# Performance work log

Measured on AMD Instinct MI355X. Metric: run time of the kernel, lower is better.

The kernel has to match this reference:

```python
import jax, jax.numpy as jnp
import numpy as np

N_NODES = 50000
N_EDGES = 800000
N_GRAPHS = 512
EPS = 1e-5
SLOPE = 0.2  # LeakyReLU negative slope in GATv2


def setup_inputs() -> dict:
    key = jax.random.key(0)
    ks = jax.random.split(key, 20)
    s = 0.1
    inp = {
        "x": jax.random.normal(ks[0], (N_NODES, 9), jnp.float32),
        "edge_attr": jax.random.normal(ks[1], (N_EDGES, 3), jnp.float32),
        "Wl0": jax.random.normal(ks[2], (9, 64), jnp.float32) * s,
        "Wr0": jax.random.normal(ks[3], (9, 64), jnp.float32) * s,
        "bl0": jnp.zeros((64,), jnp.float32),
        "br0": jnp.zeros((64,), jnp.float32),
        "We0": jax.random.normal(ks[4], (3, 64), jnp.float32) * s,
        "att0": jax.random.normal(ks[5], (64,), jnp.float32) * s,
        "bo0": jnp.zeros((64,), jnp.float32),
        "Wl": jax.random.normal(ks[6], (4, 64, 64), jnp.float32) * s,
        "Wr": jax.random.normal(ks[7], (4, 64, 64), jnp.float32) * s,
        "bl": jnp.zeros((4, 64), jnp.float32),
        "br": jnp.zeros((4, 64), jnp.float32),
        "We": jax.random.normal(ks[8], (4, 3, 64), jnp.float32) * s,
        "att": jax.random.normal(ks[9], (4, 64), jnp.float32) * s,
        "bo": jnp.zeros((4, 64), jnp.float32),
        "bn_g": jnp.ones((5, 64), jnp.float32),
        "bn_b": jnp.zeros((5, 64), jnp.float32),
        "bn_m": jnp.zeros((5, 64), jnp.float32),
        "bn_v": jax.random.uniform(ks[10], (5, 64), jnp.float32, 0.5, 1.5),
        "Wjk": jax.random.normal(ks[11], (64, 64), jnp.float32) * s,
        "bjk": jnp.zeros((64,), jnp.float32),
        "Whead": jax.random.normal(ks[12], (64, 1), jnp.float32) * s,
        "bhead": jnp.zeros((1,), jnp.float32),
        "edge_index": jax.random.randint(ks[13], (2, N_EDGES), 0, N_NODES, jnp.int32),
        "batch": jnp.sort(jax.random.randint(ks[14], (N_NODES,), 0, N_GRAPHS, jnp.int32)),
        "num_graphs": N_GRAPHS,
    }
    return inp


def gatv2_layer(h, src, dst, ea, Wl_, bl_, Wr_, br_, We_, a_, bo_, n_nodes):
    # GATv2Conv (heads=1, edge_dim) : e_ij = a . LeakyReLU(Wl h_j + Wr h_i + We e_ij)
    xl = h @ Wl_ + bl_                          # [N, 64] source transform
    xr = h @ Wr_ + br_                          # [N, 64] dest transform
    e = jax.nn.leaky_relu(xl[src] + xr[dst] + ea @ We_, SLOPE)  # [E, 64]
    logit = e @ a_                              # [E]
    m = jax.ops.segment_max(logit, dst, num_segments=n_nodes)
    m = jnp.where(jnp.isfinite(m), m, 0.0)      # empty segments -> -inf
    p = jnp.exp(logit - m[dst])
    z = jax.ops.segment_sum(p, dst, num_segments=n_nodes)
    alpha = p / jnp.maximum(z[dst], 1e-16)      # softmax over in-edges of dst
    out = jax.ops.segment_sum(alpha[:, None] * xl[src], dst, num_segments=n_nodes)
    return out + bo_


def bn_relu(h, g, b, m, v):
    # eval-mode BatchNorm1d followed by ReLU (BasicGNN: norm then act)
    return jax.nn.relu((h - m) * (g * jax.lax.rsqrt(v + EPS)) + b)


def reference(x, edge_attr, Wl0, Wr0, bl0, br0, We0, att0, bo0,
              Wl, Wr, bl, br, We, att, bo,
              bn_g, bn_b, bn_m, bn_v, Wjk, bjk, Whead, bhead,
              edge_index, batch, num_graphs):
    n = x.shape[0]
    src, dst = edge_index[0], edge_index[1]
    h = gatv2_layer(x, src, dst, edge_attr, Wl0, bl0, Wr0, br0, We0, att0, bo0, n)
    h = bn_relu(h, bn_g[0], bn_b[0], bn_m[0], bn_v[0])
    for i in range(4):
        h = gatv2_layer(h, src, dst, edge_attr, Wl[i], bl[i], Wr[i], br[i], We[i], att[i], bo[i], n)
        h = bn_relu(h, bn_g[i + 1], bn_b[i + 1], bn_m[i + 1], bn_v[i + 1])
    h = h @ Wjk + bjk                            # jk='last' output projection 64->64
    # global mean pool over graphs
    sums = jax.ops.segment_sum(h, batch, num_segments=num_graphs)          # [G, 64]
    cnt = jax.ops.segment_sum(jnp.ones((n,), h.dtype), batch, num_segments=num_graphs)
    pooled = sums / jnp.maximum(cnt, 1.0)[:, None]
    return pooled @ Whead + bhead                # [G, 1]  (dropout inactive in eval)
```

## Files before the change

### kernel.cpp

```cpp
#include <hip/hip_runtime.h>
#include <math.h>

#define N_NODES 50000
#define N_EDGES 800000
#define N_GRAPHS 512
#define SLOPE 0.2f
#define CAP 48
static constexpr float EPS_BN = 1e-5f;

typedef float v2f __attribute__((ext_vector_type(2)));


__global__ __launch_bounds__(256) void scatter_t10_kernel(
    const int* __restrict__ src, const int* __restrict__ dst,
    const float* __restrict__ ea,
    int* __restrict__ cnt, float4* __restrict__ rec,
    const float* __restrict__ x,
    const float* __restrict__ Wl0, const float* __restrict__ bl0,
    const float* __restrict__ Wr0, const float* __restrict__ br0,
    float* __restrict__ xl, float* __restrict__ xr) {
    int t = threadIdx.x;
    int e0 = blockIdx.x * 512 + t;
    int e1 = e0 + 256;
    bool v0 = e0 < N_EDGES;
    bool v1 = e1 < N_EDGES;
    int ec0 = v0 ? e0 : 0;
    int ec1 = v1 ? e1 : 0;
    int d0 = dst[ec0];
    int d1 = dst[ec1];
    int s0 = src[ec0];
    int s1 = src[ec1];
    float a00 = ea[ec0 * 3 + 0], a01 = ea[ec0 * 3 + 1], a02 = ea[ec0 * 3 + 2];
    float a10 = ea[ec1 * 3 + 0], a11 = ea[ec1 * 3 + 1], a12 = ea[ec1 * 3 + 2];
    int p0 = v0 ? atomicAdd(&cnt[d0], 1) : CAP;
    int p1 = v1 ? atomicAdd(&cnt[d1], 1) : CAP;
    if (v0 && p0 < CAP)
        rec[(size_t)d0 * CAP + p0] = make_float4(__int_as_float(s0 * 64), a00, a01, a02);
    if (v1 && p1 < CAP)
        rec[(size_t)d1 * CAP + p1] = make_float4(__int_as_float(s1 * 64), a10, a11, a12);

    int w = t >> 6;
    int k = t & 63;
    v2f wlr[9];
#pragma unroll
    for (int j = 0; j < 9; j++) wlr[j] = (v2f){Wl0[j * 64 + k], Wr0[j * 64 + k]};
    v2f bias = {bl0[k], br0[k]};
    const int NW = gridDim.x * 4;
    for (int n = blockIdx.x * 4 + w; n < N_NODES; n += NW) {
        int un = __builtin_amdgcn_readfirstlane(n);
        const float* __restrict__ hrow = x + (size_t)un * 9;
        float hb[9];
#pragma unroll
        for (int j = 0; j < 9; j++) hb[j] = hrow[j];
        v2f acc = bias;
#pragma unroll
        for (int j = 0; j < 9; j++)
            acc = __builtin_elementwise_fma((v2f){hb[j], hb[j]}, wlr[j], acc);
        xl[(size_t)un * 64 + k] = acc.x;
        xr[(size_t)un * 64 + k] = acc.y;
    }
}


__global__ __launch_bounds__(256) void transform6_kernel(
    const float* __restrict__ h,
    const float* __restrict__ Wl, const float* __restrict__ bl,
    const float* __restrict__ Wr, const float* __restrict__ br,
    float* __restrict__ xl, float* __restrict__ xr) {
    __shared__ float sAt[64][68];
    __shared__ float sB[64][128];
    int t = threadIdx.x;
    int n0 = blockIdx.x * 64;

#pragma unroll
    for (int i = 0; i < 4; i++) {
        int idx = i * 256 + t;
        int row = idx >> 4;
        int fc  = idx & 15;
        int n = n0 + row;
        float4 v = (n < N_NODES) ? *((const float4*)(h + (size_t)n * 64 + fc * 4))
                                 : make_float4(0.f, 0.f, 0.f, 0.f);
        sAt[fc * 4 + 0][row] = v.x;
        sAt[fc * 4 + 1][row] = v.y;
        sAt[fc * 4 + 2][row] = v.z;
        sAt[fc * 4 + 3][row] = v.w;
    }
#pragma unroll
    for (int i = 0; i < 8; i++) {
        int idx = i * 256 + t;
        int j  = idx >> 5;
        int fc = idx & 31;
        int c  = fc * 4;
        float4 v = (c < 64) ? *((const float4*)(Wl + j * 64 + c))
                            : *((const float4*)(Wr + j * 64 + (c - 64)));
        *((float4*)&sB[j][c]) = v;
    }
    __syncthreads();

    int tx = t & 15, ty = t >> 4;
    int c0 = tx * 4;
    float4 bls = *((const float4*)(bl + c0));
    float4 brs = *((const float4*)(br + c0));
    v2f acc[4][4];
#pragma unroll
    for (int r = 0; r < 4; r++) {
        acc[r][0] = (v2f){bls.x, bls.y};
        acc[r][1] = (v2f){bls.z, bls.w};
        acc[r][2] = (v2f){brs.x, brs.y};
        acc[r][3] = (v2f){brs.z, brs.w};
    }

#pragma unroll 4
    for (int j = 0; j < 64; j++) {
        float a0 = sAt[j][ty * 4 + 0];
        float a1 = sAt[j][ty * 4 + 1];
        float a2 = sAt[j][ty * 4 + 2];
        float a3 = sAt[j][ty * 4 + 3];
        float4 bq0 = *((const float4*)&sB[j][c0]);
        float4 bq1 = *((const float4*)&sB[j][64 + c0]);
        v2f b0 = {bq0.x, bq0.y}, b1 = {bq0.z, bq0.w};
        v2f b2 = {bq1.x, bq1.y}, b3 = {bq1.z, bq1.w};
        v2f a0v = {a0, a0}, a1v = {a1, a1}, a2v = {a2, a2}, a3v = {a3, a3};
        acc[0][0] = __builtin_elementwise_fma(a0v, b0, acc[0][0]);
        acc[0][1] = __builtin_elementwise_fma(a0v, b1, acc[0][1]);
        acc[0][2] = __builtin_elementwise_fma(a0v, b2, acc[0][2]);
        acc[0][3] = __builtin_elementwise_fma(a0v, b3, acc[0][3]);
        acc[1][0] = __builtin_elementwise_fma(a1v, b0, acc[1][0]);
        acc[1][1] = __builtin_elementwise_fma(a1v, b1, acc[1][1]);
        acc[1][2] = __builtin_elementwise_fma(a1v, b2, acc[1][2]);
        acc[1][3] = __builtin_elementwise_fma(a1v, b3, acc[1][3]);
        acc[2][0] = __builtin_elementwise_fma(a2v, b0, acc[2][0]);
        acc[2][1] = __builtin_elementwise_fma(a2v, b1, acc[2][1]);
        acc[2][2] = __builtin_elementwise_fma(a2v, b2, acc[2][2]);
        acc[2][3] = __builtin_elementwise_fma(a2v, b3, acc[2][3]);
        acc[3][0] = __builtin_elementwise_fma(a3v, b0, acc[3][0]);
        acc[3][1] = __builtin_elementwise_fma(a3v, b1, acc[3][1]);
        acc[3][2] = __builtin_elementwise_fma(a3v, b2, acc[3][2]);
        acc[3][3] = __builtin_elementwise_fma(a3v, b3, acc[3][3]);
    }

#pragma unroll
    for (int r = 0; r < 4; r++) {
        int n = n0 + ty * 4 + r;
        if (n < N_NODES) {
            *((float4*)(xl + (size_t)n * 64 + c0)) =
                make_float4(acc[r][0].x, acc[r][0].y, acc[r][1].x, acc[r][1].y);
            *((float4*)(xr + (size_t)n * 64 + c0)) =
                make_float4(acc[r][2].x, acc[r][2].y, acc[r][3].x, acc[r][3].y);
        }
    }
}


#define EDGE_T(rX, xXa, xXb, accX)                                        \
    {                                                                     \
        v2f tXa = xXa + xra, tXb = xXb + xrb;                             \
        tXa = __builtin_elementwise_fma((v2f){rX.y, rX.y}, we0a, tXa);    \
        tXb = __builtin_elementwise_fma((v2f){rX.y, rX.y}, we0b, tXb);    \
        tXa = __builtin_elementwise_fma((v2f){rX.z, rX.z}, we1a, tXa);    \
        tXb = __builtin_elementwise_fma((v2f){rX.z, rX.z}, we1b, tXb);    \
        tXa = __builtin_elementwise_fma((v2f){rX.w, rX.w}, we2a, tXa);    \
        tXb = __builtin_elementwise_fma((v2f){rX.w, rX.w}, we2b, tXb);    \
        tXa = __builtin_elementwise_max(tXa, tXa * SLOPE);                \
        tXb = __builtin_elementwise_max(tXb, tXb * SLOPE);                \
        v2f dX = ata * tXa;                                               \
        dX = __builtin_elementwise_fma(atb, tXb, dX);                     \
        accX = dX.x + dX.y;                                               \
    }

__global__ __launch_bounds__(256, 4) void gat_fused8_kernel(
    const float* __restrict__ xl, const float* __restrict__ xr,
    const float4* __restrict__ recP, const int* __restrict__ cnt,
    const float* __restrict__ We, const float* __restrict__ att,
    const float* __restrict__ bo,
    const float* __restrict__ bn_g, const float* __restrict__ bn_b,
    const float* __restrict__ bn_m, const float* __restrict__ bn_v,
    float* __restrict__ hout) {
    int t = threadIdx.x;
    int w = t >> 6;
    int lane = t & 63;
    int q = lane >> 4;
    int r = lane & 15;
    int k4 = r * 4;
    int n = blockIdx.x * 4 + w;

    float4 we0 = *(const float4*)(We + 0 * 64 + k4);
    float4 we1 = *(const float4*)(We + 64 + k4);
    float4 we2 = *(const float4*)(We + 128 + k4);
    float4 at4 = *(const float4*)(att + k4);
    float4 xq  = *(const float4*)(xr + (size_t)n * 64 + k4);
    v2f we0a = {we0.x, we0.y}, we0b = {we0.z, we0.w};
    v2f we1a = {we1.x, we1.y}, we1b = {we1.z, we1.w};
    v2f we2a = {we2.x, we2.y}, we2b = {we2.z, we2.w};
    v2f ata  = {at4.x, at4.y}, atb  = {at4.z, at4.w};
    v2f xra  = {xq.x, xq.y},   xrb  = {xq.z, xq.w};
    int beg = n * CAP;
    int end = beg + min(cnt[n], CAP);

    v2f oAa = {0.f, 0.f}, oAb = {0.f, 0.f};
    v2f oBa = {0.f, 0.f}, oBb = {0.f, 0.f};
    v2f oCa = {0.f, 0.f}, oCb = {0.f, 0.f};
    v2f oDa = {0.f, 0.f}, oDb = {0.f, 0.f};
    float zA = 0.f, zB = 0.f, zC = 0.f, zD = 0.f;

    for (int c = beg; c < end; c += 16) {
        int pA = c + q;      bool vA = pA < end;
        int pB = c + 4 + q;  bool vB = pB < end;
        int pC = c + 8 + q;  bool vC = pC < end;
        int pD = c + 12 + q; bool vD = pD < end;
        float4 rA = recP[vA ? pA : beg];
        float4 rB = recP[vB ? pB : beg];
        float4 rC = recP[vC ? pC : beg];
        float4 rD = recP[vD ? pD : beg];
        unsigned offA = (unsigned)__float_as_int(rA.x) + k4;
        unsigned offB = (unsigned)__float_as_int(rB.x) + k4;
        unsigned offC = (unsigned)__float_as_int(rC.x) + k4;
        unsigned offD = (unsigned)__float_as_int(rD.x) + k4;
        float4 xA = *(const float4*)(xl + offA);
        float4 xB = *(const float4*)(xl + offB);
        float4 xC = *(const float4*)(xl + offC);
        float4 xD = *(const float4*)(xl + offD);
        v2f xAa = {xA.x, xA.y}, xAb = {xA.z, xA.w};
        v2f xBa = {xB.x, xB.y}, xBb = {xB.z, xB.w};
        v2f xCa = {xC.x, xC.y}, xCb = {xC.z, xC.w};
        v2f xDa = {xD.x, xD.y}, xDb = {xD.z, xD.w};

        float accA, accB, accC, accD;
        EDGE_T(rA, xAa, xAb, accA);
        EDGE_T(rB, xBa, xBb, accB);
        EDGE_T(rC, xCa, xCb, accC);
        EDGE_T(rD, xDa, xDb, accD);

        accA += __shfl_xor(accA, 1, 64); accB += __shfl_xor(accB, 1, 64);
        accC += __shfl_xor(accC, 1, 64); accD += __shfl_xor(accD, 1, 64);
        accA += __shfl_xor(accA, 2, 64); accB += __shfl_xor(accB, 2, 64);
        accC += __shfl_xor(accC, 2, 64); accD += __shfl_xor(accD, 2, 64);
        accA += __shfl_xor(accA, 4, 64); accB += __shfl_xor(accB, 4, 64);
        accC += __shfl_xor(accC, 4, 64); accD += __shfl_xor(accD, 4, 64);
        accA += __shfl_xor(accA, 8, 64); accB += __shfl_xor(accB, 8, 64);
        accC += __shfl_xor(accC, 8, 64); accD += __shfl_xor(accD, 8, 64);

        float peA = vA ? __expf(accA) : 0.f;
        float peB = vB ? __expf(accB) : 0.f;
        float peC = vC ? __expf(accC) : 0.f;
        float peD = vD ? __expf(accD) : 0.f;
        v2f pA2 = {peA, peA}, pB2 = {peB, peB}, pC2 = {peC, peC}, pD2 = {peD, peD};
        oAa = __builtin_elementwise_fma(pA2, xAa, oAa);
        oAb = __builtin_elementwise_fma(pA2, xAb, oAb);
        oBa = __builtin_elementwise_fma(pB2, xBa, oBa);
        oBb = __builtin_elementwise_fma(pB2, xBb, oBb);
        oCa = __builtin_elementwise_fma(pC2, xCa, oCa);
        oCb = __builtin_elementwise_fma(pC2, xCb, oCb);
        oDa = __builtin_elementwise_fma(pD2, xDa, oDa);
        oDb = __builtin_elementwise_fma(pD2, xDb, oDb);
        zA += peA; zB += peB; zC += peC; zD += peD;
    }

    v2f oa = (oAa + oBa) + (oCa + oDa);
    v2f ob = (oAb + oBb) + (oCb + oDb);
    float z = (zA + zB) + (zC + zD);
    float4 o = make_float4(oa.x, oa.y, ob.x, ob.y);
    o.x += __shfl_xor(o.x, 16, 64); o.x += __shfl_xor(o.x, 32, 64);
    o.y += __shfl_xor(o.y, 16, 64); o.y += __shfl_xor(o.y, 32, 64);
    o.z += __shfl_xor(o.z, 16, 64); o.z += __shfl_xor(o.z, 32, 64);
    o.w += __shfl_xor(o.w, 16, 64); o.w += __shfl_xor(o.w, 32, 64);
    z += __shfl_xor(z, 16, 64); z += __shfl_xor(z, 32, 64);

    if (q == 0) {
        float zi = 1.0f / fmaxf(z, 1e-16f);
        float4 bo4 = *(const float4*)(bo + k4);
        float4 g4  = *(const float4*)(bn_g + k4);
        float4 b4  = *(const float4*)(bn_b + k4);
        float4 m4  = *(const float4*)(bn_m + k4);
        float4 v4  = *(const float4*)(bn_v + k4);
        float4 res;
        res.x = fmaxf((o.x * zi + bo4.x - m4.x) * (g4.x / sqrtf(v4.x + EPS_BN)) + b4.x, 0.f);
        res.y = fmaxf((o.y * zi + bo4.y - m4.y) * (g4.y / sqrtf(v4.y + EPS_BN)) + b4.y, 0.f);
        res.z = fmaxf((o.z * zi + bo4.z - m4.z) * (g4.z / sqrtf(v4.z + EPS_BN)) + b4.z, 0.f);
        res.w = fmaxf((o.w * zi + bo4.w - m4.w) * (g4.w / sqrtf(v4.w + EPS_BN)) + b4.w, 0.f);
        *(float4*)(hout + (size_t)n * 64 + k4) = res;
    }
}


__global__ __launch_bounds__(256) void pool_all2_kernel(
    const float* __restrict__ h, const int* __restrict__ batch,
    const float* __restrict__ Wjk, const float* __restrict__ bjk,
    const float* __restrict__ Whead, const float* __restrict__ bhead,
    float* __restrict__ out) {
    __shared__ float red[4][64];
    int g = blockIdx.x;
    int t = threadIdx.x;
    int k = t & 63;
    int w = t >> 6;
    int lo = 0, hi = N_NODES;
    while (lo < hi) { int mid = (lo + hi) >> 1; if (batch[mid] < g) lo = mid + 1; else hi = mid; }
    int s = lo;
    hi = N_NODES;
    while (lo < hi) { int mid = (lo + hi) >> 1; if (batch[mid] < g + 1) lo = mid + 1; else hi = mid; }
    int e = lo;

    float acc = 0.f;
    for (int n = s + w; n < e; n += 4) acc += h[(size_t)n * 64 + k];
    red[w][k] = acc;
    __syncthreads();

    if (w == 0) {
        acc = (red[0][k] + red[1][k]) + (red[2][k] + red[3][k]);
        float wc = 0.f;
        for (int j = 0; j < 64; j++) wc = fmaf(Wjk[k * 64 + j], Whead[j], wc);
        float bc = bjk[k] * Whead[k];
        for (int off = 32; off > 0; off >>= 1) bc += __shfl_xor(bc, off, 64);
        float cntf = (float)(e - s);
        acc /= fmaxf(cntf, 1.0f);
        float v = acc * wc;
        for (int off = 32; off > 0; off >>= 1) v += __shfl_xor(v, off, 64);
        if (k == 0) out[g] = v + bc + bhead[0];
    }
}


extern "C" void kernel_launch(void* const* d_in, const int* in_sizes, int n_in,
                              void* d_out, int out_size, void* d_ws, size_t ws_size,
                              hipStream_t stream) {
    const float* x     = (const float*)d_in[0];
    const float* ea    = (const float*)d_in[1];
    const float* Wl0   = (const float*)d_in[2];
    const float* Wr0   = (const float*)d_in[3];
    const float* bl0   = (const float*)d_in[4];
    const float* br0   = (const float*)d_in[5];
    const float* We0   = (const float*)d_in[6];
    const float* att0  = (const float*)d_in[7];
    const float* bo0   = (const float*)d_in[8];
    const float* Wl    = (const float*)d_in[9];
    const float* Wr    = (const float*)d_in[10];
    const float* bl    = (const float*)d_in[11];
    const float* br    = (const float*)d_in[12];
    const float* We    = (const float*)d_in[13];
    const float* att   = (const float*)d_in[14];
    const float* bo    = (const float*)d_in[15];
    const float* bn_g  = (const float*)d_in[16];
    const float* bn_b  = (const float*)d_in[17];
    const float* bn_m  = (const float*)d_in[18];
    const float* bn_v  = (const float*)d_in[19];
    const float* Wjk   = (const float*)d_in[20];
    const float* bjk   = (const float*)d_in[21];
    const float* Whead = (const float*)d_in[22];
    const float* bhead = (const float*)d_in[23];
    const int* edge_index = (const int*)d_in[24];
    const int* batch      = (const int*)d_in[25];

    const int* srcIdx = edge_index;
    const int* dstIdx = edge_index + N_EDGES;

    char* ws = (char*)d_ws;
    size_t off = 0;
    auto alloc = [&](size_t bytes) -> void* {
        void* p = ws + off;
        off += (bytes + 255) & ~(size_t)255;
        return p;
    };
    float* hA      = (float*)alloc((size_t)N_NODES * 64 * 4);
    float* hB      = (float*)alloc((size_t)N_NODES * 64 * 4);
    float* xlb     = (float*)alloc((size_t)N_NODES * 64 * 4);
    float* xrb     = (float*)alloc((size_t)N_NODES * 64 * 4);
    int*   cnt     = (int*)alloc((size_t)N_NODES * 4);
    float4* recP   = (float4*)alloc((size_t)N_NODES * CAP * 16);

    hipMemsetAsync(cnt, 0, (size_t)N_NODES * 4, stream);
    const int NSB = (N_EDGES + 511) / 512;
    scatter_t10_kernel<<<NSB, 256, 0, stream>>>(
        srcIdx, dstIdx, ea, cnt, recP, x, Wl0, bl0, Wr0, br0, xlb, xrb);

    const int NBN = N_NODES / 4;
    const int NBG = (N_NODES + 63) / 64;

    gat_fused8_kernel<<<NBN, 256, 0, stream>>>(xlb, xrb, recP, cnt,
                                               We0, att0, bo0,
                                               bn_g, bn_b, bn_m, bn_v, hA);

    float* hcur = hA;
    float* hnext = hB;
    for (int i = 0; i < 4; i++) {
        transform6_kernel<<<NBG, 256, 0, stream>>>(hcur,
            Wl + (size_t)i * 64 * 64, bl + (size_t)i * 64,
            Wr + (size_t)i * 64 * 64, br + (size_t)i * 64,
            xlb, xrb);
        gat_fused8_kernel<<<NBN, 256, 0, stream>>>(xlb, xrb, recP, cnt,
            We + (size_t)i * 3 * 64, att + (size_t)i * 64,
            bo + (size_t)i * 64,
            bn_g + (size_t)(i + 1) * 64, bn_b + (size_t)(i + 1) * 64,
            bn_m + (size_t)(i + 1) * 64, bn_v + (size_t)(i + 1) * 64,
            hnext);
        float* tp = hcur; hcur = hnext; hnext = tp;
    }

    pool_all2_kernel<<<N_GRAPHS, 256, 0, stream>>>(hcur, batch, Wjk, bjk, Whead, bhead,
                                                   (float*)d_out);
}
```

Measured before the change: 518.2 us.

## Make GAT aggregation persistent with software-prefetched edge records and hoisted BN constants

The GAT aggregation kernel becomes a grid-stride persistent kernel (2048 blocks), with one wave per node per iteration. Its edge loop drops from 4 to 2 edge groups per step, and the next step's edge records are prefetched while the current gather and compute run. BatchNorm scale and shift are folded once per thread before the node loop. The scatter kernel goes back to one edge per thread, and the occupancy hint in launch_bounds is removed. This trades memory-level parallelism per iteration for lower register use and more latency overlap.

After: 460.6 us. 11.1% less time.

```diff
diff --git a/kernel.cpp b/kernel.cpp
--- a/kernel.cpp
+++ b/kernel.cpp
@@ -11,7 +11,7 @@
 typedef float v2f __attribute__((ext_vector_type(2)));
 
 
-__global__ __launch_bounds__(256) void scatter_t10_kernel(
+__global__ __launch_bounds__(256) void scatter_t9_kernel(
     const int* __restrict__ src, const int* __restrict__ dst,
     const float* __restrict__ ea,
     int* __restrict__ cnt, float4* __restrict__ rec,
@@ -20,24 +20,14 @@
     const float* __restrict__ Wr0, const float* __restrict__ br0,
     float* __restrict__ xl, float* __restrict__ xr) {
     int t = threadIdx.x;
-    int e0 = blockIdx.x * 512 + t;
-    int e1 = e0 + 256;
-    bool v0 = e0 < N_EDGES;
-    bool v1 = e1 < N_EDGES;
-    int ec0 = v0 ? e0 : 0;
-    int ec1 = v1 ? e1 : 0;
-    int d0 = dst[ec0];
-    int d1 = dst[ec1];
-    int s0 = src[ec0];
-    int s1 = src[ec1];
-    float a00 = ea[ec0 * 3 + 0], a01 = ea[ec0 * 3 + 1], a02 = ea[ec0 * 3 + 2];
-    float a10 = ea[ec1 * 3 + 0], a11 = ea[ec1 * 3 + 1], a12 = ea[ec1 * 3 + 2];
-    int p0 = v0 ? atomicAdd(&cnt[d0], 1) : CAP;
-    int p1 = v1 ? atomicAdd(&cnt[d1], 1) : CAP;
-    if (v0 && p0 < CAP)
-        rec[(size_t)d0 * CAP + p0] = make_float4(__int_as_float(s0 * 64), a00, a01, a02);
-    if (v1 && p1 < CAP)
-        rec[(size_t)d1 * CAP + p1] = make_float4(__int_as_float(s1 * 64), a10, a11, a12);
+    int e = blockIdx.x * 256 + t;
+    if (e < N_EDGES) {
+        int d = dst[e];
+        int pos = atomicAdd(&cnt[d], 1);
+        if (pos < CAP)
+            rec[(size_t)d * CAP + pos] = make_float4(__int_as_float(src[e] * 64),
+                                                     ea[e * 3 + 0], ea[e * 3 + 1], ea[e * 3 + 2]);
+    }
 
     int w = t >> 6;
     int k = t & 63;
@@ -168,7 +158,7 @@
         accX = dX.x + dX.y;                                               \
     }
 
-__global__ __launch_bounds__(256, 4) void gat_fused8_kernel(
+__global__ __launch_bounds__(256) void gat_fused9_kernel(
     const float* __restrict__ xl, const float* __restrict__ xr,
     const float4* __restrict__ recP, const int* __restrict__ cnt,
     const float* __restrict__ We, const float* __restrict__ att,
@@ -182,103 +172,98 @@
     int q = lane >> 4;
     int r = lane & 15;
     int k4 = r * 4;
-    int n = blockIdx.x * 4 + w;
 
     float4 we0 = *(const float4*)(We + 0 * 64 + k4);
     float4 we1 = *(const float4*)(We + 64 + k4);
     float4 we2 = *(const float4*)(We + 128 + k4);
     float4 at4 = *(const float4*)(att + k4);
-    float4 xq  = *(const float4*)(xr + (size_t)n * 64 + k4);
     v2f we0a = {we0.x, we0.y}, we0b = {we0.z, we0.w};
     v2f we1a = {we1.x, we1.y}, we1b = {we1.z, we1.w};
     v2f we2a = {we2.x, we2.y}, we2b = {we2.z, we2.w};
     v2f ata  = {at4.x, at4.y}, atb  = {at4.z, at4.w};
-    v2f xra  = {xq.x, xq.y},   xrb  = {xq.z, xq.w};
-    int beg = n * CAP;
-    int end = beg + min(cnt[n], CAP);
-
-    v2f oAa = {0.f, 0.f}, oAb = {0.f, 0.f};
-    v2f oBa = {0.f, 0.f}, oBb = {0.f, 0.f};
-    v2f oCa = {0.f, 0.f}, oCb = {0.f, 0.f};
-    v2f oDa = {0.f, 0.f}, oDb = {0.f, 0.f};
-    float zA = 0.f, zB = 0.f, zC = 0.f, zD = 0.f;
-
-    for (int c = beg; c < end; c += 16) {
-        int pA = c + q;      bool vA = pA < end;
-        int pB = c + 4 + q;  bool vB = pB < end;
-        int pC = c + 8 + q;  bool vC = pC < end;
-        int pD = c + 12 + q; bool vD = pD < end;
+    float4 bo4 = *(const float4*)(bo + k4);
+    float4 g4  = *(const float4*)(bn_g + k4);
+    float4 b4  = *(const float4*)(bn_b + k4);
+    float4 m4  = *(const float4*)(bn_m + k4);
+    float4 v4  = *(const float4*)(bn_v + k4);
+    float4 S, C;
+    S.x = g4.x / sqrtf(v4.x + EPS_BN);  C.x = (bo4.x - m4.x) * S.x + b4.x;
+    S.y = g4.y / sqrtf(v4.y + EPS_BN);  C.y = (bo4.y - m4.y) * S.y + b4.y;
+    S.z = g4.z / sqrtf(v4.z + EPS_BN);  C.z = (bo4.z - m4.z) * S.z + b4.z;
+    S.w = g4.w / sqrtf(v4.w + EPS_BN);  C.w = (bo4.w - m4.w) * S.w + b4.w;
+
+    const int NW = gridDim.x * 4;
+    for (int n0 = blockIdx.x * 4 + w; n0 < N_NODES; n0 += NW) {
+        int n = __builtin_amdgcn_readfirstlane(n0);
+        float4 xq = *(const float4*)(xr + (size_t)n * 64 + k4);
+        v2f xra = {xq.x, xq.y}, xrb = {xq.z, xq.w};
+        int beg = n * CAP;
+        int end = beg + min(cnt[n], CAP);
+
+        v2f oAa = {0.f, 0.f}, oAb = {0.f, 0.f};
+        v2f oBa = {0.f, 0.f}, oBb = {0.f, 0.f};
+        float zA = 0.f, zB = 0.f;
+
+        int c = beg;
+        int pA = c + q;     bool vA = pA < end;
+        int pB = c + 4 + q; bool vB = pB < end;
         float4 rA = recP[vA ? pA : beg];
         float4 rB = recP[vB ? pB : beg];
-        float4 rC = recP[vC ? pC : beg];
-        float4 rD = recP[vD ? pD : beg];
-        unsigned offA = (unsigned)__float_as_int(rA.x) + k4;
-        unsigned offB = (unsigned)__float_as_int(rB.x) + k4;
-        unsigned offC = (unsigned)__float_as_int(rC.x) + k4;
-        unsigned offD = (unsigned)__float_as_int(rD.x) + k4;
-        float4 xA = *(const float4*)(xl + offA);
-        float4 xB = *(const float4*)(xl + offB);
-        float4 xC = *(const float4*)(xl + offC);
-        float4 xD = *(const float4*)(xl + offD);
-        v2f xAa = {xA.x, xA.y}, xAb = {xA.z, xA.w};
-        v2f xBa = {xB.x, xB.y}, xBb = {xB.z, xB.w};
-        v2f xCa = {xC.x, xC.y}, xCb = {xC.z, xC.w};
-        v2f xDa = {xD.x, xD.y}, xDb = {xD.z, xD.w};
-
-        float accA, accB, accC, accD;
-        EDGE_T(rA, xAa, xAb, accA);
-        EDGE_T(rB, xBa, xBb, accB);
-        EDGE_T(rC, xCa, xCb, accC);
-        EDGE_T(rD, xDa, xDb, accD);
-
-        accA += __shfl_xor(accA, 1, 64); accB += __shfl_xor(accB, 1, 64);
-        accC += __shfl_xor(accC, 1, 64); accD += __shfl_xor(accD, 1, 64);
-        accA += __shfl_xor(accA, 2, 64); accB += __shfl_xor(accB, 2, 64);
-        accC += __shfl_xor(accC, 2, 64); accD += __shfl_xor(accD, 2, 64);
-        accA += __shfl_xor(accA, 4, 64); accB += __shfl_xor(accB, 4, 64);
-        accC += __shfl_xor(accC, 4, 64); accD += __shfl_xor(accD, 4, 64);
-        accA += __shfl_xor(accA, 8, 64); accB += __shfl_xor(accB, 8, 64);
-        accC += __shfl_xor(accC, 8, 64); accD += __shfl_xor(accD, 8, 64);
-
-        float peA = vA ? __expf(accA) : 0.f;
-        float peB = vB ? __expf(accB) : 0.f;
-        float peC = vC ? __expf(accC) : 0.f;
-        float peD = vD ? __expf(accD) : 0.f;
-        v2f pA2 = {peA, peA}, pB2 = {peB, peB}, pC2 = {peC, peC}, pD2 = {peD, peD};
-        oAa = __builtin_elementwise_fma(pA2, xAa, oAa);
-        oAb = __builtin_elementwise_fma(pA2, xAb, oAb);
-        oBa = __builtin_elementwise_fma(pB2, xBa, oBa);
-        oBb = __builtin_elementwise_fma(pB2, xBb, oBb);
-        oCa = __builtin_elementwise_fma(pC2, xCa, oCa);
-        oCb = __builtin_elementwise_fma(pC2, xCb, oCb);
-        oDa = __builtin_elementwise_fma(pD2, xDa, oDa);
-        oDb = __builtin_elementwise_fma(pD2, xDb, oDb);
-        zA += peA; zB += peB; zC += peC; zD += peD;
-    }
-
-    v2f oa = (oAa + oBa) + (oCa + oDa);
-    v2f ob = (oAb + oBb) + (oCb + oDb);
-    float z = (zA + zB) + (zC + zD);
-    float4 o = make_float4(oa.x, oa.y, ob.x, ob.y);
-    o.x += __shfl_xor(o.x, 16, 64); o.x += __shfl_xor(o.x, 32, 64);
-    o.y += __shfl_xor(o.y, 16, 64); o.y += __shfl_xor(o.y, 32, 64);
-    o.z += __shfl_xor(o.z, 16, 64); o.z += __shfl_xor(o.z, 32, 64);
-    o.w += __shfl_xor(o.w, 16, 64); o.w += __shfl_xor(o.w, 32, 64);
-    z += __shfl_xor(z, 16, 64); z += __shfl_xor(z, 32, 64);
-
-    if (q == 0) {
-        float zi = 1.0f / fmaxf(z, 1e-16f);
-        float4 bo4 = *(const float4*)(bo + k4);
-        float4 g4  = *(const float4*)(bn_g + k4);
-        float4 b4  = *(const float4*)(bn_b + k4);
-        float4 m4  = *(const float4*)(bn_m + k4);
-        float4 v4  = *(const float4*)(bn_v + k4);
-        float4 res;
-        res.x = fmaxf((o.x * zi + bo4.x - m4.x) * (g4.x / sqrtf(v4.x + EPS_BN)) + b4.x, 0.f);
-        res.y = fmaxf((o.y * zi + bo4.y - m4.y) * (g4.y / sqrtf(v4.y + EPS_BN)) + b4.y, 0.f);
-        res.z = fmaxf((o.z * zi + bo4.z - m4.z) * (g4.z / sqrtf(v4.z + EPS_BN)) + b4.z, 0.f);
-        res.w = fmaxf((o.w * zi + bo4.w - m4.w) * (g4.w / sqrtf(v4.w + EPS_BN)) + b4.w, 0.f);
-        *(float4*)(hout + (size_t)n * 64 + k4) = res;
+
+        while (c < end) {
+            unsigned offA = (unsigned)__float_as_int(rA.x) + k4;
+            unsigned offB = (unsigned)__float_as_int(rB.x) + k4;
+            float4 xA = *(const float4*)(xl + offA);
+            float4 xB = *(const float4*)(xl + offB);
+
+            int c2 = c + 8;
+            int pA2 = c2 + q;     bool vA2 = pA2 < end;
+            int pB2 = c2 + 4 + q; bool vB2 = pB2 < end;
+            float4 rA2 = recP[vA2 ? pA2 : beg];
+            float4 rB2 = recP[vB2 ? pB2 : beg];
+
+            v2f xAa = {xA.x, xA.y}, xAb = {xA.z, xA.w};
+            v2f xBa = {xB.x, xB.y}, xBb = {xB.z, xB.w};
+
+            float accA, accB;
+            EDGE_T(rA, xAa, xAb, accA);
+            EDGE_T(rB, xBa, xBb, accB);
+
+            accA += __shfl_xor(accA, 1, 64);  accB += __shfl_xor(accB, 1, 64);
+            accA += __shfl_xor(accA, 2, 64);  accB += __shfl_xor(accB, 2, 64);
+            accA += __shfl_xor(accA, 4, 64);  accB += __shfl_xor(accB, 4, 64);
+            accA += __shfl_xor(accA, 8, 64);  accB += __shfl_xor(accB, 8, 64);
+
+            float peA = vA ? __expf(accA) : 0.f;
+            float peB = vB ? __expf(accB) : 0.f;
+            v2f pA2v = {peA, peA}, pB2v = {peB, peB};
+            oAa = __builtin_elementwise_fma(pA2v, xAa, oAa);
+            oAb = __builtin_elementwise_fma(pA2v, xAb, oAb);
+            oBa = __builtin_elementwise_fma(pB2v, xBa, oBa);
+            oBb = __builtin_elementwise_fma(pB2v, xBb, oBb);
+            zA += peA; zB += peB;
+
+            rA = rA2; rB = rB2; vA = vA2; vB = vB2; c = c2;
+        }
+
+        v2f oa = oAa + oBa, ob = oAb + oBb;
+        float z = zA + zB;
+        float4 o = make_float4(oa.x, oa.y, ob.x, ob.y);
+        o.x += __shfl_xor(o.x, 16, 64); o.x += __shfl_xor(o.x, 32, 64);
+        o.y += __shfl_xor(o.y, 16, 64); o.y += __shfl_xor(o.y, 32, 64);
+        o.z += __shfl_xor(o.z, 16, 64); o.z += __shfl_xor(o.z, 32, 64);
+        o.w += __shfl_xor(o.w, 16, 64); o.w += __shfl_xor(o.w, 32, 64);
+        z += __shfl_xor(z, 16, 64); z += __shfl_xor(z, 32, 64);
+
+        if (q == 0) {
+            float zi = 1.0f / fmaxf(z, 1e-16f);
+            float4 res;
+            res.x = fmaxf(fmaf(o.x * zi, S.x, C.x), 0.f);
+            res.y = fmaxf(fmaf(o.y * zi, S.y, C.y), 0.f);
+            res.z = fmaxf(fmaf(o.z * zi, S.z, C.z), 0.f);
+            res.w = fmaxf(fmaf(o.w * zi, S.w, C.w), 0.f);
+            *(float4*)(hout + (size_t)n * 64 + k4) = res;
+        }
     }
 }
 
@@ -368,16 +353,15 @@
     float4* recP   = (float4*)alloc((size_t)N_NODES * CAP * 16);
 
     hipMemsetAsync(cnt, 0, (size_t)N_NODES * 4, stream);
-    const int NSB = (N_EDGES + 511) / 512;
-    scatter_t10_kernel<<<NSB, 256, 0, stream>>>(
+    scatter_t9_kernel<<<(N_EDGES + 255) / 256, 256, 0, stream>>>(
         srcIdx, dstIdx, ea, cnt, recP, x, Wl0, bl0, Wr0, br0, xlb, xrb);
 
-    const int NBN = N_NODES / 4;
+    const int GB  = 2048;
     const int NBG = (N_NODES + 63) / 64;
 
-    gat_fused8_kernel<<<NBN, 256, 0, stream>>>(xlb, xrb, recP, cnt,
-                                               We0, att0, bo0,
-                                               bn_g, bn_b, bn_m, bn_v, hA);
+    gat_fused9_kernel<<<GB, 256, 0, stream>>>(xlb, xrb, recP, cnt,
+                                              We0, att0, bo0,
+                                              bn_g, bn_b, bn_m, bn_v, hA);
 
     float* hcur = hA;
     float* hnext = hB;
@@ -386,7 +370,7 @@
             Wl + (size_t)i * 64 * 64, bl + (size_t)i * 64,
             Wr + (size_t)i * 64 * 64, br + (size_t)i * 64,
             xlb, xrb);
-        gat_fused8_kernel<<<NBN, 256, 0, stream>>>(xlb, xrb, recP, cnt,
+        gat_fused9_kernel<<<GB, 256, 0, stream>>>(xlb, xrb, recP, cnt,
             We + (size_t)i * 3 * 64, att + (size_t)i * 64,
             bo + (size_t)i * 64,
             bn_g + (size_t)(i + 1) * 64, bn_b + (size_t)(i + 1) * 64,
```
